# Performance work log

Hardware: AMD Instinct MI355X
Metric: run time of the kernel (lower is better)

The kernel has to match this reference:

```python
import jax, jax.numpy as jnp
import numpy as np

N_GROUPS = 32  # getGroupSize(.) assumed -> channels // 8 (or //24 for 3*ch) == 32 for ch=256
HEADS = 4


def group_norm(x, gamma, beta, groups=N_GROUPS, eps=1e-5):
    n, c = x.shape
    xg = x.reshape(n, groups, c // groups)
    mu = xg.mean(-1, keepdims=True)
    var = xg.var(-1, keepdims=True)
    xn = ((xg - mu) * jax.lax.rsqrt(var + eps)).reshape(n, c)
    return xn * gamma + beta


def setup_inputs():
    key = jax.random.key(0)
    N, E, CH, HID = 2000, 16000, 256, 256
    ks = jax.random.split(key, 24)

    def w(k, shape, s=0.02):
        return (jax.random.normal(k, shape) * s).astype(jnp.float32)

    inp = {
        'x': jax.random.normal(ks[0], (N, CH), jnp.float32),
        'edge_index': jax.random.randint(ks[1], (2, E), 0, N),
        'edge_attr': jax.random.normal(ks[2], (E, CH), jnp.float32),
        # edge_mlp: GN(3ch)+ReLU -> Linear(3ch,hid) -> GN(hid)+ReLU -> Linear(hid,ch)
        'gn_e1_g': jnp.ones((3 * CH,), jnp.float32), 'gn_e1_b': jnp.zeros((3 * CH,), jnp.float32),
        'We1': w(ks[3], (3 * CH, HID)), 'be1': jnp.zeros((HID,), jnp.float32),
        'gn_e2_g': jnp.ones((HID,), jnp.float32), 'gn_e2_b': jnp.zeros((HID,), jnp.float32),
        'We2': w(ks[4], (HID, CH)), 'be2': jnp.zeros((CH,), jnp.float32),
        # actN: GN(ch)+ReLU
        'gn_n_g': jnp.ones((CH,), jnp.float32), 'gn_n_b': jnp.zeros((CH,), jnp.float32),
        # multi-head attention projections
        'Wq': w(ks[5], (CH, CH)), 'bq': jnp.zeros((CH,), jnp.float32),
        'Wk': w(ks[6], (CH, CH)), 'bk': jnp.zeros((CH,), jnp.float32),
        'Wv': w(ks[7], (CH, CH)), 'bv': jnp.zeros((CH,), jnp.float32),
        'Wo': w(ks[8], (CH, CH)), 'bo': jnp.zeros((CH,), jnp.float32),
        # node_mlp: Linear(2ch,hid) -> GN(hid)+ReLU -> Linear(hid,ch)
        'Wn1': w(ks[9], (2 * CH, HID)), 'bn1': jnp.zeros((HID,), jnp.float32),
        'gn_n2_g': jnp.ones((HID,), jnp.float32), 'gn_n2_b': jnp.zeros((HID,), jnp.float32),
        'Wn2': w(ks[10], (HID, CH)), 'bn2': jnp.zeros((CH,), jnp.float32),
    }
    return inp


def reference(x, edge_index, edge_attr,
              gn_e1_g, gn_e1_b, We1, be1, gn_e2_g, gn_e2_b, We2, be2,
              gn_n_g, gn_n_b, Wq, bq, Wk, bk, Wv, bv, Wo, bo,
              Wn1, bn1, gn_n2_g, gn_n2_b, Wn2, bn2):
    row, col = edge_index[0], edge_index[1]
    N, ch = x.shape
    E = edge_attr.shape[0]
    dk = ch // HEADS

    # ---- edge model: cat(src, tgt, e) -> GN/ReLU -> Lin -> GN/ReLU -> Lin (+res) ----
    e_in = jnp.concatenate([x[row], x[col], edge_attr], axis=1)  # [E, 3ch]
    h = jax.nn.relu(group_norm(e_in, gn_e1_g, gn_e1_b))
    h = h @ We1 + be1
    h = jax.nn.relu(group_norm(h, gn_e2_g, gn_e2_b))
    e_out = h @ We2 + be2 + edge_attr  # [E, ch]

    # ---- node model: dense-masked MHA, queries=nodes, keys/values=edges ----
    mask = jnp.zeros((N, E), x.dtype).at[col, jnp.arange(E)].set(1.0)  # scatter adjacency
    q = (x @ Wq + bq).reshape(N, HEADS, dk)
    k = (e_out @ Wk + bk).reshape(E, HEADS, dk)
    v = (e_out @ Wv + bv).reshape(E, HEADS, dk)
    scores = jnp.einsum('nhd,ehd->hne', q, k) / jnp.sqrt(jnp.float32(dk))  # [H, N, E]
    scores = jnp.where(mask[None] > 0, scores, jnp.float32(-1e9))
    attn = jax.nn.softmax(scores, axis=-1)
    g = jnp.einsum('hne,ehd->nhd', attn, v).reshape(N, ch) @ Wo + bo  # [N, ch]

    xa = jax.nn.relu(group_norm(x, gn_n_g, gn_n_b))
    h = jnp.concatenate([xa, g], axis=1) @ Wn1 + bn1  # thinker='cat'
    h = jax.nn.relu(group_norm(h, gn_n2_g, gn_n2_b))
    n_out = h @ Wn2 + bn2 + x  # residual

    return n_out, e_out
```

## Files before the change

### kernel.cpp

```cpp
#include <hip/hip_runtime.h>
#include <hip/hip_bf16.h>
#include <stdint.h>
#include <math.h>

#define CH 256

typedef __attribute__((ext_vector_type(8)))  short short8;
typedef __attribute__((ext_vector_type(16))) short short16;
typedef __attribute__((ext_vector_type(4)))  float f32x4;

#define GL2LDS16(g, l) __builtin_amdgcn_global_load_lds(                       \
    (const __attribute__((address_space(1))) void*)(g),                        \
    (__attribute__((address_space(3))) void*)(l), 16, 0, 0)

__device__ inline short f2bf(float f) {
    __hip_bfloat16 h = __float2bfloat16(f);
    short s;
    __builtin_memcpy(&s, &h, 2);
    return s;
}

__device__ inline float bf2f(short s) {
    unsigned u = ((unsigned)(unsigned short)s) << 16;
    float f;
    __builtin_memcpy(&f, &u, 4);
    return f;
}

__device__ inline float warp_sum64(float v) {
    v += __shfl_xor(v, 32, 64);
    v += __shfl_xor(v, 16, 64);
    v += __shfl_xor(v, 8, 64);
    v += __shfl_xor(v, 4, 64);
    v += __shfl_xor(v, 2, 64);
    v += __shfl_xor(v, 1, 64);
    return v;
}

__device__ inline float warp_max64(float v) {
    v = fmaxf(v, __shfl_xor(v, 32, 64));
    v = fmaxf(v, __shfl_xor(v, 16, 64));
    v = fmaxf(v, __shfl_xor(v, 8, 64));
    v = fmaxf(v, __shfl_xor(v, 4, 64));
    v = fmaxf(v, __shfl_xor(v, 2, 64));
    v = fmaxf(v, __shfl_xor(v, 1, 64));
    return v;
}

struct GArgs {
    const short* A; const short* Bt; const float* bias; const float* res;
    float* C; short* Cbf;
    const float* gamma; const float* beta; float* vbar;
    int M, K, Nc, ldc, coff;
    const short* A2; const short* Bt2; const float* bias2; short* Cbf2;
    int M2, Nc2, y_split;
    const short* xbf; const short* eabf; const int* rowi; const int* coli;
    const float* mu; const float* rs; const float* vg; const float* vbt;
    int* cursor; int* elist;
    const int* counts; int* offsets; int Nn;
};

template <int BM, int BN, int AMODE, int EPI, int DUAL, int VB, int FILL,
          int SCAN = 0, int PAN2 = 0>
__global__ __launch_bounds__(256) void mfma_gemm(GArgs g)
{
    constexpr int BK = 64;
    constexpr int AK = AMODE ? (BK + 8) : BK;
    constexpr int HM = BM / 2, HN = BN / 2;
    constexpr int FM = HM / 16, FN = HN / 16;
    constexpr int PA = BM / 32;
    constexpr int PB = BN / 32;
    constexpr int NP2 = PAN2 ? 2 : 1;
    __shared__ short As[BM * AK];
    __shared__ short Bs[NP2 * BN * BK];
    __shared__ int sidx[AMODE ? 2 * BM : 1];

    const short* A = g.A; const short* Bt = g.Bt;
    const float* bias = g.bias; const float* res = g.res;
    float* C = g.C; short* Cbf = g.Cbf;
    int M = g.M, ldc = g.ldc, co = g.coff;
    const int K = g.K;
    int by = blockIdx.y, bx = blockIdx.x;

    if constexpr (SCAN) {
        if (by == (int)gridDim.y - 1) {
            const int t0 = threadIdx.x;
            if (bx == 0) {
                int* ss = (int*)As;
                int base8 = t0 * 8;
                int loc[8]; int srun = 0;
                #pragma unroll
                for (int j = 0; j < 8; j++) {
                    int idx = base8 + j;
                    int c = (idx < g.Nn) ? g.counts[idx] : 0;
                    loc[j] = srun; srun += c;
                }
                ss[t0] = srun;
                __syncthreads();
                for (int off = 1; off < 256; off <<= 1) {
                    int v = (t0 >= off) ? ss[t0 - off] : 0;
                    __syncthreads();
                    ss[t0] += v;
                    __syncthreads();
                }
                int excl = (t0 > 0) ? ss[t0 - 1] : 0;
                #pragma unroll
                for (int j = 0; j < 8; j++) {
                    int idx = base8 + j;
                    if (idx < g.Nn) {
                        int v = excl + loc[j];
                        g.offsets[idx] = v;
                        g.cursor[idx]  = v;
                    }
                }
                if (t0 == 255) g.offsets[g.Nn] = ss[255];
            }
            return;
        }
    }

    bool qrole = false;
    if constexpr (DUAL) {
        if (by >= g.y_split) {
            by -= g.y_split;
            if (bx * BN >= g.Nc2) return;
            qrole = true;
            A = g.A2; Bt = g.Bt2; bias = g.bias2; Cbf = g.Cbf2;
            C = nullptr; res = nullptr;
            M = g.M2; ldc = g.Nc2; co = 0;
        }
    }

    const int t = threadIdx.x;
    const int wave = t >> 6, lane = t & 63;
    const int q = lane >> 4, l16 = lane & 15;
    const int row0 = by * BM;
    const int col0 = bx * BN;
    const int wm = wave & 1, wn = wave >> 1;

    if constexpr (AMODE) {
        if (t < BM) {
            int gr = row0 + t; if (gr >= M) gr = M - 1;
            sidx[t] = g.rowi[gr];
            sidx[BM + t] = g.coli[gr];
        }
        __syncthreads();
    }

    if constexpr (FILL) {
        if (!qrole && bx == 0 && t < BM) {
            int rg = row0 + t;
            if (rg < M) {
                int c = g.coli[rg];
                int p = atomicAdd(&g.cursor[c], 1);
                g.elist[p] = rg;
            }
        }
    }

    f32x4 acc[NP2][FM][FN];
    #pragma unroll
    for (int p2 = 0; p2 < NP2; p2++)
        #pragma unroll
        for (int i = 0; i < FM; i++)
            #pragma unroll
            for (int j = 0; j < FN; j++) acc[p2][i][j] = (f32x4){0.f, 0.f, 0.f, 0.f};

    for (int k0 = 0; k0 < K; k0 += BK) {
        if constexpr (AMODE == 1) {
            int reg = k0 >> 8;
            int rloc = t >> 3;
            int c8 = (t & 7) * 8;
            int pos = k0 + c8;
            int G = pos / 24;
            float4 ga  = *(const float4*)&g.vg[pos];
            float4 ga2 = *(const float4*)&g.vg[pos + 4];
            float4 gb  = *(const float4*)&g.vbt[pos];
            float4 gb2 = *(const float4*)&g.vbt[pos + 4];
            int off = pos & 255;
            #pragma unroll
            for (int p = 0; p < BM / 32; p++) {
                int r2 = p * 32 + rloc;
                int e = row0 + r2; if (e >= M) e = M - 1;
                const short* srow;
                if (reg == 0)      srow = g.xbf + (size_t)sidx[r2] * CH;
                else if (reg == 1) srow = g.xbf + (size_t)sidx[BM + r2] * CH;
                else               srow = g.eabf + (size_t)e * CH;
                short8 v8 = *(const short8*)&srow[off];
                float mm = g.mu[(size_t)e * 32 + G];
                float rr = g.rs[(size_t)e * 32 + G];
                short8 o;
                o[0] = f2bf(fmaxf((bf2f(v8[0]) - mm) * rr * ga.x + gb.x, 0.f));
                o[1] = f2bf(fmaxf((bf2f(v8[1]) - mm) * rr * ga.y + gb.y, 0.f));
                o[2] = f2bf(fmaxf((bf2f(v8[2]) - mm) * rr * ga.z + gb.z, 0.f));
                o[3] = f2bf(fmaxf((bf2f(v8[3]) - mm) * rr * ga.w + gb.w, 0.f));
                o[4] = f2bf(fmaxf((bf2f(v8[4]) - mm) * rr * ga2.x + gb2.x, 0.f));
                o[5] = f2bf(fmaxf((bf2f(v8[5]) - mm) * rr * ga2.y + gb2.y, 0.f));
                o[6] = f2bf(fmaxf((bf2f(v8[6]) - mm) * rr * ga2.z + gb2.z, 0.f));
                o[7] = f2bf(fmaxf((bf2f(v8[7]) - mm) * rr * ga2.w + gb2.w, 0.f));
                *(short8*)&As[r2 * AK + c8] = o;
            }
        } else {
            #pragma unroll
            for (int p = 0; p < PA; p++) {
                int chunk = p * 256 + t;
                int r = chunk >> 3;
                int cs = (((chunk & 7) ^ (r & 7)) * 8);
                int gr = row0 + r; if (gr >= M) gr = M - 1;
                const short* gsrc = A + (size_t)gr * K + k0 + cs;
                short* ldst = &As[(p * 256 + wave * 64) * 8];
                GL2LDS16(gsrc, ldst);
            }
        }
        #pragma unroll
        for (int p2 = 0; p2 < NP2; p2++) {
            if (!(PAN2 && p2 == 1 && qrole)) {
                #pragma unroll
                for (int p = 0; p < PB; p++) {
                    int chunk = p * 256 + t;
                    int r = chunk >> 3;
                    int cs = (((chunk & 7) ^ (r & 7)) * 8);
                    const short* gsrc = Bt + (size_t)(col0 + p2 * 256 + r) * K + k0 + cs;
                    short* ldst = &Bs[p2 * BN * BK + (p * 256 + wave * 64) * 8];
                    GL2LDS16(gsrc, ldst);
                }
            }
        }
        __syncthreads();
        #pragma unroll
        for (int ks = 0; ks < 2; ks++) {
            short8 af[FM];
            #pragma unroll
            for (int mi = 0; mi < FM; mi++) {
                int R = wm * HM + mi * 16 + l16;
                if constexpr (AMODE == 1)
                    af[mi] = *(const short8*)&As[R * AK + ks * 32 + q * 8];
                else {
                    int slot = ((ks * 4 + q) ^ (R & 7)) * 8;
                    af[mi] = *(const short8*)&As[R * BK + slot];
                }
            }
            #pragma unroll
            for (int p2 = 0; p2 < NP2; p2++) {
                if (!(PAN2 && p2 == 1 && qrole)) {
                    short8 bfr[FN];
                    #pragma unroll
                    for (int ni = 0; ni < FN; ni++) {
                        int R = wn * HN + ni * 16 + l16;
                        int slot = ((ks * 4 + q) ^ (R & 7)) * 8;
                        bfr[ni] = *(const short8*)&Bs[p2 * BN * BK + R * BK + slot];
                    }
                    #pragma unroll
                    for (int mi = 0; mi < FM; mi++)
                        #pragma unroll
                        for (int ni = 0; ni < FN; ni++)
                            acc[p2][mi][ni] = __builtin_amdgcn_mfma_f32_16x16x32_bf16(
                                af[mi], bfr[ni], acc[p2][mi][ni], 0, 0, 0);
                }
            }
        }
        __syncthreads();
    }

    #pragma unroll
    for (int p2 = 0; p2 < NP2; p2++) {
        if (PAN2 && p2 == 1 && qrole) continue;
        #pragma unroll
        for (int ni = 0; ni < FN; ni++) {
            int cg = col0 + p2 * 256 + wn * HN + ni * 16 + l16;
            float bv = bias[cg];
            if constexpr (EPI == 1) {
                float ga = g.gamma[cg], be = g.beta[cg];
                #pragma unroll
                for (int mi = 0; mi < FM; mi++) {
                    #pragma unroll
                    for (int r = 0; r < 4; r++) {
                        float v = acc[p2][mi][ni][r] + bv;
                        float s = v, sq = v * v;
                        s += __shfl_xor(s, 1, 64);  sq += __shfl_xor(sq, 1, 64);
                        s += __shfl_xor(s, 2, 64);  sq += __shfl_xor(sq, 2, 64);
                        s += __shfl_xor(s, 4, 64);  sq += __shfl_xor(sq, 4, 64);
                        float mean = s * 0.125f;
                        float var = sq * 0.125f - mean * mean;
                        float o = fmaxf((v - mean) * rsqrtf(var + 1e-5f) * ga + be, 0.f);
                        int rg = row0 + wm * HM + mi * 16 + q * 4 + r;
                        if (rg < M) Cbf[(size_t)rg * ldc + co + cg] = f2bf(o);
                    }
                }
            } else {
                #pragma unroll
                for (int mi = 0; mi < FM; mi++) {
                    #pragma unroll
                    for (int r = 0; r < 4; r++) {
                        int rg = row0 + wm * HM + mi * 16 + q * 4 + r;
                        if (rg < M) {
                            float v = acc[p2][mi][ni][r] + bv;
                            if (res) v += res[(size_t)rg * ldc + co + cg];
                            if (C)   C[(size_t)rg * ldc + co + cg] = v;
                            if (Cbf) Cbf[(size_t)rg * ldc + co + cg] = f2bf(v);
                        }
                    }
                }
                if constexpr (VB) {
                    bool vpanel = PAN2 ? (p2 == 1) : (!qrole && cg >= 256);
                    if (vpanel) {
                        float part = 0.f;
                        #pragma unroll
                        for (int mi = 0; mi < FM; mi++)
                            #pragma unroll
                            for (int r = 0; r < 4; r++) {
                                int rg = row0 + wm * HM + mi * 16 + q * 4 + r;
                                if (rg < M) part += acc[p2][mi][ni][r] + bv;
                            }
                        part += __shfl_xor(part, 16, 64);
                        part += __shfl_xor(part, 32, 64);
                        if (q == 0) atomicAdd(&g.vbar[cg - 256], part);
                    }
                }
            }
        }
    }
}

struct PrepPack {
    const float* wsrc[8];
    short* wdst[8];
    int wK[8];
    int wstart[8];
    int NW, NP;
    const float* x;
    short* x_bf;
    short* cat_bf;
    float2* xs;
    const float* gng;
    const float* gnb;
    float* vbar;
    const float* bk;
    const float* bv;
    float* bkv;
    int* counts;
    int N;
};

__global__ __launch_bounds__(256) void prep_kernel(PrepPack p)
{
    int bid = blockIdx.x;
    int t = threadIdx.x;
    if (bid < p.NW) {
        int m = 0;
        #pragma unroll
        for (int i = 1; i < 8; i++) if (bid >= p.wstart[i]) m = i;
        int k0 = (bid - p.wstart[m]) * 16;
        const float* src = p.wsrc[m];
        short16 o;
        #pragma unroll
        for (int j = 0; j < 16; j++) o[j] = f2bf(src[(size_t)(k0 + j) * 256 + t]);
        *(short16*)(p.wdst[m] + (size_t)t * p.wK[m] + k0) = o;
        return;
    }
    if (bid >= p.NW + p.NP) {
        int i = (bid - p.NW - p.NP) * 256 + t;
        if (i < p.N) p.counts[i] = 0;
        return;
    }
    int pb = bid - p.NW;
    if (pb == 0) {
        p.vbar[t] = 0.f;
        p.bkv[t] = p.bk[t];
        p.bkv[256 + t] = p.bv[t];
    }
    int r = pb * 8 + (t >> 5);
    int g = t & 31;
    if (r >= p.N) return;
    size_t xb = (size_t)r * CH + g * 8;
    float4 a = *(const float4*)&p.x[xb];
    float4 b = *(const float4*)&p.x[xb + 4];
    short8 xr;
    xr[0] = f2bf(a.x); xr[1] = f2bf(a.y); xr[2] = f2bf(a.z); xr[3] = f2bf(a.w);
    xr[4] = f2bf(b.x); xr[5] = f2bf(b.y); xr[6] = f2bf(b.z); xr[7] = f2bf(b.w);
    *(short8*)&p.x_bf[xb] = xr;
    float s  = a.x + a.y + a.z + a.w + b.x + b.y + b.z + b.w;
    float s2 = a.x*a.x + a.y*a.y + a.z*a.z + a.w*a.w
             + b.x*b.x + b.y*b.y + b.z*b.z + b.w*b.w;
    p.xs[(size_t)r * 32 + g] = make_float2(s, s2);
    float m = s * 0.125f;
    float var = s2 * 0.125f - m * m;
    float rsd = rsqrtf(var + 1e-5f);
    float4 g0 = *(const float4*)&p.gng[g * 8];
    float4 g1 = *(const float4*)&p.gng[g * 8 + 4];
    float4 b0 = *(const float4*)&p.gnb[g * 8];
    float4 b1 = *(const float4*)&p.gnb[g * 8 + 4];
    short8 o;
    o[0] = f2bf(fmaxf((a.x - m) * rsd * g0.x + b0.x, 0.f));
    o[1] = f2bf(fmaxf((a.y - m) * rsd * g0.y + b0.y, 0.f));
    o[2] = f2bf(fmaxf((a.z - m) * rsd * g0.z + b0.z, 0.f));
    o[3] = f2bf(fmaxf((a.w - m) * rsd * g0.w + b0.w, 0.f));
    o[4] = f2bf(fmaxf((b.x - m) * rsd * g1.x + b1.x, 0.f));
    o[5] = f2bf(fmaxf((b.y - m) * rsd * g1.y + b1.y, 0.f));
    o[6] = f2bf(fmaxf((b.z - m) * rsd * g1.z + b1.z, 0.f));
    o[7] = f2bf(fmaxf((b.w - m) * rsd * g1.w + b1.w, 0.f));
    *(short8*)&p.cat_bf[(size_t)r * (2 * CH) + g * 8] = o;
}

__global__ __launch_bounds__(256) void estats_kernel(
    const float* __restrict__ eattr, const int* __restrict__ rowi,
    const int* __restrict__ coli, const float2* __restrict__ xs,
    float* __restrict__ mu, float* __restrict__ rs,
    short* __restrict__ eabf, int* __restrict__ counts, int E)
{
    __shared__ float2 ea[8][32];
    int t = threadIdx.x;
    int slot = t >> 5, g = t & 31;
    int e = blockIdx.x * 8 + slot;
    float4 a = *(const float4*)&eattr[(size_t)e * CH + g * 8];
    float4 b = *(const float4*)&eattr[(size_t)e * CH + g * 8 + 4];
    short8 o8;
    o8[0] = f2bf(a.x); o8[1] = f2bf(a.y); o8[2] = f2bf(a.z); o8[3] = f2bf(a.w);
    o8[4] = f2bf(b.x); o8[5] = f2bf(b.y); o8[6] = f2bf(b.z); o8[7] = f2bf(b.w);
    *(short8*)&eabf[(size_t)e * CH + g * 8] = o8;
    float s  = a.x + a.y + a.z + a.w + b.x + b.y + b.z + b.w;
    float s2 = a.x*a.x + a.y*a.y + a.z*a.z + a.w*a.w
             + b.x*b.x + b.y*b.y + b.z*b.z + b.w*b.w;
    ea[slot][g] = make_float2(s, s2);
    int r = rowi[e], c = coli[e];
    if (g == 0) atomicAdd(&counts[c], 1);
    __syncthreads();
    float S = 0.f, S2 = 0.f;
    #pragma unroll
    for (int j = 0; j < 3; j++) {
        int b3 = 3 * g + j;
        int src = b3 >> 5, idx = b3 & 31;
        float2 v;
        if (src == 0)      v = xs[(size_t)r * 32 + idx];
        else if (src == 1) v = xs[(size_t)c * 32 + idx];
        else               v = ea[slot][idx];
        S += v.x; S2 += v.y;
    }
    float m = S * (1.f / 24.f);
    float var = S2 * (1.f / 24.f) - m * m;
    mu[(size_t)e * 32 + g] = m;
    rs[(size_t)e * 32 + g] = rsqrtf(var + 1e-5f);
}

__global__ __launch_bounds__(256) void attn_kernel(
    const short* __restrict__ qb, const short* __restrict__ kvb,
    const int* __restrict__ offsets, const int* __restrict__ elist,
    const float* __restrict__ vbar, short* __restrict__ g_bf, int N, int E)
{
    __shared__ int eidx[64];
    __shared__ float scl[4 * 64];
    int n = blockIdx.x;
    int wave = threadIdx.x >> 6;
    int lane = threadIdx.x & 63;
    int s0 = offsets[n], s1 = offsets[n + 1];
    float q0 = bf2f(qb[(size_t)n * CH + lane]);
    float q1 = bf2f(qb[(size_t)n * CH + 64 + lane]);
    float q2 = bf2f(qb[(size_t)n * CH + 128 + lane]);
    float q3 = bf2f(qb[(size_t)n * CH + 192 + lane]);
    float out = 0.f, m = -INFINITY, l = 0.f;
    for (int base = s0; base < s1; base += 64) {
        int cn = s1 - base; if (cn > 64) cn = 64;
        if (wave == 0 && lane < cn) eidx[lane] = elist[base + lane];
        __syncthreads();
        for (int j = wave; j < cn; j += 4) {
            int e = eidx[j];
            const short* kr = kvb + (size_t)e * 512;
            float d0 = warp_sum64(q0 * bf2f(kr[lane]));
            float d1 = warp_sum64(q1 * bf2f(kr[64 + lane]));
            float d2 = warp_sum64(q2 * bf2f(kr[128 + lane]));
            float d3 = warp_sum64(q3 * bf2f(kr[192 + lane]));
            if (lane == 0) {
                scl[j]       = d0 * 0.125f;
                scl[64 + j]  = d1 * 0.125f;
                scl[128 + j] = d2 * 0.125f;
                scl[192 + j] = d3 * 0.125f;
            }
        }
        __syncthreads();
        float s = (lane < cn) ? scl[wave * 64 + lane] : -INFINITY;
        float mc = warp_max64(s);
        float nm = fmaxf(m, mc);
        float scale = __expf(m - nm);
        float pp = (lane < cn) ? __expf(s - nm) : 0.f;
        float ps = warp_sum64(pp);
        l = l * scale + ps;
        out *= scale;
        m = nm;
        for (int i = 0; i < cn; i++) {
            float pi = __shfl(pp, i, 64);
            int ei = eidx[i];
            out += pi * bf2f(kvb[(size_t)ei * 512 + 256 + wave * 64 + lane]);
        }
        __syncthreads();
    }
    float res;
    if (s1 > s0) res = out / l;
    else         res = vbar[wave * 64 + lane] * (1.f / (float)E);
    g_bf[(size_t)n * CH + wave * 64 + lane] = f2bf(res);
}

extern "C" void kernel_launch(void* const* d_in, const int* in_sizes, int n_in,
                              void* d_out, int out_size, void* d_ws, size_t ws_size,
                              hipStream_t stream)
{
    const float* x       = (const float*)d_in[0];
    const int*   ei      = (const int*)d_in[1];
    const float* eattr   = (const float*)d_in[2];
    const float* gn_e1_g = (const float*)d_in[3];
    const float* gn_e1_b = (const float*)d_in[4];
    const float* We1     = (const float*)d_in[5];
    const float* be1     = (const float*)d_in[6];
    const float* gn_e2_g = (const float*)d_in[7];
    const float* gn_e2_b = (const float*)d_in[8];
    const float* We2     = (const float*)d_in[9];
    const float* be2     = (const float*)d_in[10];
    const float* gn_n_g  = (const float*)d_in[11];
    const float* gn_n_b  = (const float*)d_in[12];
    const float* Wq      = (const float*)d_in[13];
    const float* bq      = (const float*)d_in[14];
    const float* Wk      = (const float*)d_in[15];
    const float* bk      = (const float*)d_in[16];
    const float* Wv      = (const float*)d_in[17];
    const float* bv      = (const float*)d_in[18];
    const float* Wo      = (const float*)d_in[19];
    const float* bo      = (const float*)d_in[20];
    const float* Wn1     = (const float*)d_in[21];
    const float* bn1     = (const float*)d_in[22];
    const float* gn_n2_g = (const float*)d_in[23];
    const float* gn_n2_b = (const float*)d_in[24];
    const float* Wn2     = (const float*)d_in[25];
    const float* bn2     = (const float*)d_in[26];

    const int N = in_sizes[0] / CH;
    const int E = in_sizes[2] / CH;

    float* nout = (float*)d_out;
    float* eout = (float*)d_out + (size_t)N * CH;

    char* base = (char*)d_ws;
    short* kv_bf  = (short*)base; base += (size_t)E * 512 * 2;
    short* h2_bf  = (short*)base; base += (size_t)E * CH * 2;
    short* eo_bf  = (short*)base; base += (size_t)E * CH * 2;
    short* eabf   = (short*)base; base += (size_t)E * CH * 2;
    short* q_bf   = (short*)base; base += (size_t)N * CH * 2;
    short* g_bf   = (short*)base; base += (size_t)N * CH * 2;
    short* cat_bf = (short*)base; base += (size_t)N * 2 * CH * 2;
    short* hn_bf  = (short*)base; base += (size_t)N * CH * 2;
    short* x_bf   = (short*)base; base += (size_t)N * CH * 2;
    float2* xs    = (float2*)base; base += (size_t)N * 32 * 8;
    float* mub    = (float*)base; base += (size_t)E * 32 * 4;
    float* rsb    = (float*)base; base += (size_t)E * 32 * 4;
    float* vbar   = (float*)base; base += 1024;
    float* bkv    = (float*)base; base += 2048;
    short* We1t = (short*)base; base += (size_t)768 * 256 * 2;
    short* We2t = (short*)base; base += (size_t)256 * 256 * 2;
    short* Wqt  = (short*)base; base += (size_t)256 * 256 * 2;
    short* Wkvt = (short*)base; base += (size_t)512 * 256 * 2;
    short* Wot  = (short*)base; base += (size_t)256 * 256 * 2;
    short* Wn1t = (short*)base; base += (size_t)512 * 256 * 2;
    short* Wn2t = (short*)base; base += (size_t)256 * 256 * 2;
    int* counts  = (int*)base;
    int* offsets = counts + N;
    int* cursor  = offsets + (N + 1) + 3;
    int* elist   = cursor + N;

    const int* rowi = ei;
    const int* coli = ei + E;

    dim3 blk(256);

    PrepPack pp;
    const float* wsrc[8] = {We1, We2, Wq, Wk, Wv, Wo, Wn1, Wn2};
    short* wdst[8] = {We1t, We2t, Wqt, Wkvt, Wkvt + (size_t)256 * 256, Wot, Wn1t, Wn2t};
    const int wKd[8] = {768, 256, 256, 256, 256, 256, 512, 256};
    int acc = 0;
    for (int i = 0; i < 8; i++) {
        pp.wsrc[i] = wsrc[i]; pp.wdst[i] = wdst[i]; pp.wK[i] = wKd[i];
        pp.wstart[i] = acc; acc += wKd[i] / 16;
    }
    pp.NW = acc;
    pp.NP = (N + 7) / 8;
    pp.x = x; pp.x_bf = x_bf; pp.cat_bf = cat_bf; pp.xs = xs;
    pp.gng = gn_n_g; pp.gnb = gn_n_b;
    pp.vbar = vbar; pp.bk = bk; pp.bv = bv; pp.bkv = bkv;
    pp.counts = counts; pp.N = N;
    int nzero = (N + 255) / 256;
    prep_kernel<<<pp.NW + pp.NP + nzero, blk, 0, stream>>>(pp);

    estats_kernel<<<E / 8, blk, 0, stream>>>(eattr, rowi, coli, xs, mub, rsb,
                                             eabf, counts, E);

    GArgs ga = {};
    ga.Bt = We1t; ga.bias = be1; ga.Cbf = h2_bf;
    ga.gamma = gn_e2_g; ga.beta = gn_e2_b;
    ga.M = E; ga.K = 3 * CH; ga.Nc = CH; ga.ldc = CH; ga.coff = 0;
    ga.xbf = x_bf; ga.eabf = eabf; ga.rowi = rowi; ga.coli = coli;
    ga.mu = mub; ga.rs = rsb; ga.vg = gn_e1_g; ga.vbt = gn_e1_b;
    ga.counts = counts; ga.offsets = offsets; ga.cursor = cursor; ga.Nn = N;
    mfma_gemm<64, 64, 1, 1, 0, 0, 0, 1, 0><<<dim3(4, E / 64 + 1), blk, 0, stream>>>(ga);

    ga = {};
    ga.A = h2_bf; ga.Bt = We2t; ga.bias = be2; ga.res = eattr;
    ga.C = eout; ga.Cbf = eo_bf;
    ga.M = E; ga.K = CH; ga.Nc = CH; ga.ldc = CH; ga.coff = 0;
    mfma_gemm<64, 64, 0, 0, 0, 0, 0><<<dim3(4, E / 64), blk, 0, stream>>>(ga);

    ga = {};
    ga.A = eo_bf; ga.Bt = Wkvt; ga.bias = bkv; ga.Cbf = kv_bf; ga.vbar = vbar;
    ga.M = E; ga.K = CH; ga.Nc = 512; ga.ldc = 512; ga.coff = 0;
    ga.A2 = x_bf; ga.Bt2 = Wqt; ga.bias2 = bq; ga.Cbf2 = q_bf;
    ga.M2 = N; ga.Nc2 = CH; ga.y_split = E / 64;
    ga.coli = coli; ga.cursor = cursor; ga.elist = elist;
    mfma_gemm<64, 64, 0, 0, 1, 1, 1, 0, 1><<<dim3(4, E / 64 + (N + 63) / 64), blk, 0, stream>>>(ga);

    attn_kernel<<<N, blk, 0, stream>>>(q_bf, kv_bf, offsets, elist, vbar, g_bf, N, E);

    ga = {};
    ga.A = g_bf; ga.Bt = Wot; ga.bias = bo; ga.Cbf = cat_bf;
    ga.M = N; ga.K = CH; ga.Nc = CH; ga.ldc = 2 * CH; ga.coff = CH;
    mfma_gemm<32, 64, 0, 0, 0, 0, 0><<<dim3(4, (N + 31) / 32), blk, 0, stream>>>(ga);

    ga = {};
    ga.A = cat_bf; ga.Bt = Wn1t; ga.bias = bn1; ga.Cbf = hn_bf;
    ga.gamma = gn_n2_g; ga.beta = gn_n2_b;
    ga.M = N; ga.K = 2 * CH; ga.Nc = CH; ga.ldc = CH; ga.coff = 0;
    mfma_gemm<32, 64, 0, 1, 0, 0, 0><<<dim3(4, (N + 31) / 32), blk, 0, stream>>>(ga);

    ga = {};
    ga.A = hn_bf; ga.Bt = Wn2t; ga.bias = bn2; ga.res = x; ga.C = nout;
    ga.M = N; ga.K = CH; ga.Nc = CH; ga.ldc = CH; ga.coff = 0;
    mfma_gemm<32, 64, 0, 0, 0, 0, 0><<<dim3(4, (N + 31) / 32), blk, 0, stream>>>(ga);
}
```

Baseline: 238.1 us.

## Materialize normalized edge concat in stats kernel instead of gathering inside GEMM

Moves the gather of x[row], x[col] and edge_attr, plus the first GroupNorm+ReLU, out of the first edge GEMM's A-tile loader and into the edge stats kernel. The stats kernel now writes a bf16 [E,768] normalized input, and the GEMM loads it with the standard async global-to-LDS swizzled path. This drops the per-k-tile register-path gather and normalization from the GEMM and removes the mu/rs buffers. In exchange it writes and rereads a larger E*768 bf16 intermediate, about 24MB of extra traffic.

```diff
diff --git a/kernel.cpp b/kernel.cpp
--- a/kernel.cpp
+++ b/kernel.cpp
@@ -54,26 +54,23 @@
     int M, K, Nc, ldc, coff;
     const short* A2; const short* Bt2; const float* bias2; short* Cbf2;
     int M2, Nc2, y_split;
-    const short* xbf; const short* eabf; const int* rowi; const int* coli;
-    const float* mu; const float* rs; const float* vg; const float* vbt;
+    const int* coli;
     int* cursor; int* elist;
     const int* counts; int* offsets; int Nn;
 };
 
-template <int BM, int BN, int AMODE, int EPI, int DUAL, int VB, int FILL,
+template <int BM, int BN, int EPI, int DUAL, int VB, int FILL,
           int SCAN = 0, int PAN2 = 0>
 __global__ __launch_bounds__(256) void mfma_gemm(GArgs g)
 {
     constexpr int BK = 64;
-    constexpr int AK = AMODE ? (BK + 8) : BK;
     constexpr int HM = BM / 2, HN = BN / 2;
     constexpr int FM = HM / 16, FN = HN / 16;
     constexpr int PA = BM / 32;
     constexpr int PB = BN / 32;
     constexpr int NP2 = PAN2 ? 2 : 1;
-    __shared__ short As[BM * AK];
+    __shared__ short As[BM * BK];
     __shared__ short Bs[NP2 * BN * BK];
-    __shared__ int sidx[AMODE ? 2 * BM : 1];
 
     const short* A = g.A; const short* Bt = g.Bt;
     const float* bias = g.bias; const float* res = g.res;
@@ -138,15 +135,6 @@
     const int col0 = bx * BN;
     const int wm = wave & 1, wn = wave >> 1;
 
-    if constexpr (AMODE) {
-        if (t < BM) {
-            int gr = row0 + t; if (gr >= M) gr = M - 1;
-            sidx[t] = g.rowi[gr];
-            sidx[BM + t] = g.coli[gr];
-        }
-        __syncthreads();
-    }
-
     if constexpr (FILL) {
         if (!qrole && bx == 0 && t < BM) {
             int rg = row0 + t;
@@ -167,50 +155,15 @@
             for (int j = 0; j < FN; j++) acc[p2][i][j] = (f32x4){0.f, 0.f, 0.f, 0.f};
 
     for (int k0 = 0; k0 < K; k0 += BK) {
-        if constexpr (AMODE == 1) {
-            int reg = k0 >> 8;
-            int rloc = t >> 3;
-            int c8 = (t & 7) * 8;
-            int pos = k0 + c8;
-            int G = pos / 24;
-            float4 ga  = *(const float4*)&g.vg[pos];
-            float4 ga2 = *(const float4*)&g.vg[pos + 4];
-            float4 gb  = *(const float4*)&g.vbt[pos];
-            float4 gb2 = *(const float4*)&g.vbt[pos + 4];
-            int off = pos & 255;
-            #pragma unroll
-            for (int p = 0; p < BM / 32; p++) {
-                int r2 = p * 32 + rloc;
-                int e = row0 + r2; if (e >= M) e = M - 1;
-                const short* srow;
-                if (reg == 0)      srow = g.xbf + (size_t)sidx[r2] * CH;
-                else if (reg == 1) srow = g.xbf + (size_t)sidx[BM + r2] * CH;
-                else               srow = g.eabf + (size_t)e * CH;
-                short8 v8 = *(const short8*)&srow[off];
-                float mm = g.mu[(size_t)e * 32 + G];
-                float rr = g.rs[(size_t)e * 32 + G];
-                short8 o;
-                o[0] = f2bf(fmaxf((bf2f(v8[0]) - mm) * rr * ga.x + gb.x, 0.f));
-                o[1] = f2bf(fmaxf((bf2f(v8[1]) - mm) * rr * ga.y + gb.y, 0.f));
-                o[2] = f2bf(fmaxf((bf2f(v8[2]) - mm) * rr * ga.z + gb.z, 0.f));
-                o[3] = f2bf(fmaxf((bf2f(v8[3]) - mm) * rr * ga.w + gb.w, 0.f));
-                o[4] = f2bf(fmaxf((bf2f(v8[4]) - mm) * rr * ga2.x + gb2.x, 0.f));
-                o[5] = f2bf(fmaxf((bf2f(v8[5]) - mm) * rr * ga2.y + gb2.y, 0.f));
-                o[6] = f2bf(fmaxf((bf2f(v8[6]) - mm) * rr * ga2.z + gb2.z, 0.f));
-                o[7] = f2bf(fmaxf((bf2f(v8[7]) - mm) * rr * ga2.w + gb2.w, 0.f));
-                *(short8*)&As[r2 * AK + c8] = o;
-            }
-        } else {
-            #pragma unroll
-            for (int p = 0; p < PA; p++) {
-                int chunk = p * 256 + t;
-                int r = chunk >> 3;
-                int cs = (((chunk & 7) ^ (r & 7)) * 8);
-                int gr = row0 + r; if (gr >= M) gr = M - 1;
-                const short* gsrc = A + (size_t)gr * K + k0 + cs;
-                short* ldst = &As[(p * 256 + wave * 64) * 8];
-                GL2LDS16(gsrc, ldst);
-            }
+        #pragma unroll
+        for (int p = 0; p < PA; p++) {
+            int chunk = p * 256 + t;
+            int r = chunk >> 3;
+            int cs = (((chunk & 7) ^ (r & 7)) * 8);
+            int gr = row0 + r; if (gr >= M) gr = M - 1;
+            const short* gsrc = A + (size_t)gr * K + k0 + cs;
+            short* ldst = &As[(p * 256 + wave * 64) * 8];
+            GL2LDS16(gsrc, ldst);
         }
         #pragma unroll
         for (int p2 = 0; p2 < NP2; p2++) {
@@ -233,12 +186,8 @@
             #pragma unroll
             for (int mi = 0; mi < FM; mi++) {
                 int R = wm * HM + mi * 16 + l16;
-                if constexpr (AMODE == 1)
-                    af[mi] = *(const short8*)&As[R * AK + ks * 32 + q * 8];
-                else {
-                    int slot = ((ks * 4 + q) ^ (R & 7)) * 8;
-                    af[mi] = *(const short8*)&As[R * BK + slot];
-                }
+                int slot = ((ks * 4 + q) ^ (R & 7)) * 8;
+                af[mi] = *(const short8*)&As[R * BK + slot];
             }
             #pragma unroll
             for (int p2 = 0; p2 < NP2; p2++) {
@@ -405,19 +354,17 @@
 __global__ __launch_bounds__(256) void estats_kernel(
     const float* __restrict__ eattr, const int* __restrict__ rowi,
     const int* __restrict__ coli, const float2* __restrict__ xs,
-    float* __restrict__ mu, float* __restrict__ rs,
-    short* __restrict__ eabf, int* __restrict__ counts, int E)
+    const short* __restrict__ x_bf,
+    const float* __restrict__ g1v, const float* __restrict__ b1v,
+    short* __restrict__ e1n, int* __restrict__ counts, int E)
 {
     __shared__ float2 ea[8][32];
+    __shared__ float2 musr[8][32];
     int t = threadIdx.x;
     int slot = t >> 5, g = t & 31;
     int e = blockIdx.x * 8 + slot;
     float4 a = *(const float4*)&eattr[(size_t)e * CH + g * 8];
     float4 b = *(const float4*)&eattr[(size_t)e * CH + g * 8 + 4];
-    short8 o8;
-    o8[0] = f2bf(a.x); o8[1] = f2bf(a.y); o8[2] = f2bf(a.z); o8[3] = f2bf(a.w);
-    o8[4] = f2bf(b.x); o8[5] = f2bf(b.y); o8[6] = f2bf(b.z); o8[7] = f2bf(b.w);
-    *(short8*)&eabf[(size_t)e * CH + g * 8] = o8;
     float s  = a.x + a.y + a.z + a.w + b.x + b.y + b.z + b.w;
     float s2 = a.x*a.x + a.y*a.y + a.z*a.z + a.w*a.w
              + b.x*b.x + b.y*b.y + b.z*b.z + b.w*b.w;
@@ -438,8 +385,37 @@
     }
     float m = S * (1.f / 24.f);
     float var = S2 * (1.f / 24.f) - m * m;
-    mu[(size_t)e * 32 + g] = m;
-    rs[(size_t)e * 32 + g] = rsqrtf(var + 1e-5f);
+    musr[slot][g] = make_float2(m, rsqrtf(var + 1e-5f));
+    __syncthreads();
+    #pragma unroll
+    for (int seg = 0; seg < 3; seg++) {
+        int pos = seg * 256 + g * 8;
+        float2 ms = musr[slot][pos / 24];
+        float4 ga  = *(const float4*)&g1v[pos];
+        float4 ga2 = *(const float4*)&g1v[pos + 4];
+        float4 gb  = *(const float4*)&b1v[pos];
+        float4 gb2 = *(const float4*)&b1v[pos + 4];
+        float v0, v1, v2, v3, v4, v5, v6, v7;
+        if (seg == 2) {
+            v0 = a.x; v1 = a.y; v2 = a.z; v3 = a.w;
+            v4 = b.x; v5 = b.y; v6 = b.z; v7 = b.w;
+        } else {
+            const short* srow = x_bf + (size_t)(seg == 0 ? r : c) * CH + g * 8;
+            short8 v8 = *(const short8*)srow;
+            v0 = bf2f(v8[0]); v1 = bf2f(v8[1]); v2 = bf2f(v8[2]); v3 = bf2f(v8[3]);
+            v4 = bf2f(v8[4]); v5 = bf2f(v8[5]); v6 = bf2f(v8[6]); v7 = bf2f(v8[7]);
+        }
+        short8 o;
+        o[0] = f2bf(fmaxf((v0 - ms.x) * ms.y * ga.x  + gb.x,  0.f));
+        o[1] = f2bf(fmaxf((v1 - ms.x) * ms.y * ga.y  + gb.y,  0.f));
+        o[2] = f2bf(fmaxf((v2 - ms.x) * ms.y * ga.z  + gb.z,  0.f));
+        o[3] = f2bf(fmaxf((v3 - ms.x) * ms.y * ga.w  + gb.w,  0.f));
+        o[4] = f2bf(fmaxf((v4 - ms.x) * ms.y * ga2.x + gb2.x, 0.f));
+        o[5] = f2bf(fmaxf((v5 - ms.x) * ms.y * ga2.y + gb2.y, 0.f));
+        o[6] = f2bf(fmaxf((v6 - ms.x) * ms.y * ga2.z + gb2.z, 0.f));
+        o[7] = f2bf(fmaxf((v7 - ms.x) * ms.y * ga2.w + gb2.w, 0.f));
+        *(short8*)&e1n[(size_t)e * 768 + pos] = o;
+    }
 }
 
 __global__ __launch_bounds__(256) void attn_kernel(
@@ -541,15 +517,13 @@
     short* kv_bf  = (short*)base; base += (size_t)E * 512 * 2;
     short* h2_bf  = (short*)base; base += (size_t)E * CH * 2;
     short* eo_bf  = (short*)base; base += (size_t)E * CH * 2;
-    short* eabf   = (short*)base; base += (size_t)E * CH * 2;
+    short* e1n    = (short*)base; base += (size_t)E * 768 * 2;
     short* q_bf   = (short*)base; base += (size_t)N * CH * 2;
     short* g_bf   = (short*)base; base += (size_t)N * CH * 2;
     short* cat_bf = (short*)base; base += (size_t)N * 2 * CH * 2;
     short* hn_bf  = (short*)base; base += (size_t)N * CH * 2;
     short* x_bf   = (short*)base; base += (size_t)N * CH * 2;
     float2* xs    = (float2*)base; base += (size_t)N * 32 * 8;
-    float* mub    = (float*)base; base += (size_t)E * 32 * 4;
-    float* rsb    = (float*)base; base += (size_t)E * 32 * 4;
     float* vbar   = (float*)base; base += 1024;
     float* bkv    = (float*)base; base += 2048;
     short* We1t = (short*)base; base += (size_t)768 * 256 * 2;
@@ -587,23 +561,21 @@
     int nzero = (N + 255) / 256;
     prep_kernel<<<pp.NW + pp.NP + nzero, blk, 0, stream>>>(pp);
 
-    estats_kernel<<<E / 8, blk, 0, stream>>>(eattr, rowi, coli, xs, mub, rsb,
-                                             eabf, counts, E);
+    estats_kernel<<<E / 8, blk, 0, stream>>>(eattr, rowi, coli, xs, x_bf,
+                                             gn_e1_g, gn_e1_b, e1n, counts, E);
 
     GArgs ga = {};
-    ga.Bt = We1t; ga.bias = be1; ga.Cbf = h2_bf;
+    ga.A = e1n; ga.Bt = We1t; ga.bias = be1; ga.Cbf = h2_bf;
     ga.gamma = gn_e2_g; ga.beta = gn_e2_b;
     ga.M = E; ga.K = 3 * CH; ga.Nc = CH; ga.ldc = CH; ga.coff = 0;
-    ga.xbf = x_bf; ga.eabf = eabf; ga.rowi = rowi; ga.coli = coli;
-    ga.mu = mub; ga.rs = rsb; ga.vg = gn_e1_g; ga.vbt = gn_e1_b;
     ga.counts = counts; ga.offsets = offsets; ga.cursor = cursor; ga.Nn = N;
-    mfma_gemm<64, 64, 1, 1, 0, 0, 0, 1, 0><<<dim3(4, E / 64 + 1), blk, 0, stream>>>(ga);
+    mfma_gemm<64, 64, 1, 0, 0, 0, 1, 0><<<dim3(4, E / 64 + 1), blk, 0, stream>>>(ga);
 
     ga = {};
     ga.A = h2_bf; ga.Bt = We2t; ga.bias = be2; ga.res = eattr;
     ga.C = eout; ga.Cbf = eo_bf;
     ga.M = E; ga.K = CH; ga.Nc = CH; ga.ldc = CH; ga.coff = 0;
-    mfma_gemm<64, 64, 0, 0, 0, 0, 0><<<dim3(4, E / 64), blk, 0, stream>>>(ga);
+    mfma_gemm<64, 64, 0, 0, 0, 0><<<dim3(4, E / 64), blk, 0, stream>>>(ga);
 
     ga = {};
     ga.A = eo_bf; ga.Bt = Wkvt; ga.bias = bkv; ga.Cbf = kv_bf; ga.vbar = vbar;
@@ -611,23 +583,23 @@
     ga.A2 = x_bf; ga.Bt2 = Wqt; ga.bias2 = bq; ga.Cbf2 = q_bf;
     ga.M2 = N; ga.Nc2 = CH; ga.y_split = E / 64;
     ga.coli = coli; ga.cursor = cursor; ga.elist = elist;
-    mfma_gemm<64, 64, 0, 0, 1, 1, 1, 0, 1><<<dim3(4, E / 64 + (N + 63) / 64), blk, 0, stream>>>(ga);
+    mfma_gemm<64, 64, 0, 1, 1, 1, 0, 1><<<dim3(4, E / 64 + (N + 63) / 64), blk, 0, stream>>>(ga);
 
     attn_kernel<<<N, blk, 0, stream>>>(q_bf, kv_bf, offsets, elist, vbar, g_bf, N, E);
 
     ga = {};
     ga.A = g_bf; ga.Bt = Wot; ga.bias = bo; ga.Cbf = cat_bf;
     ga.M = N; ga.K = CH; ga.Nc = CH; ga.ldc = 2 * CH; ga.coff = CH;
-    mfma_gemm<32, 64, 0, 0, 0, 0, 0><<<dim3(4, (N + 31) / 32), blk, 0, stream>>>(ga);
+    mfma_gemm<32, 64, 0, 0, 0, 0><<<dim3(4, (N + 31) / 32), blk, 0, stream>>>(ga);
 
     ga = {};
     ga.A = cat_bf; ga.Bt = Wn1t; ga.bias = bn1; ga.Cbf = hn_bf;
     ga.gamma = gn_n2_g; ga.beta = gn_n2_b;
     ga.M = N; ga.K = 2 * CH; ga.Nc = CH; ga.ldc = CH; ga.coff = 0;
-    mfma_gemm<32, 64, 0, 1, 0, 0, 0><<<dim3(4, (N + 31) / 32), blk, 0, stream>>>(ga);
+    mfma_gemm<32, 64, 1, 0, 0, 0><<<dim3(4, (N + 31) / 32), blk, 0, stream>>>(ga);
 
     ga = {};
     ga.A = hn_bf; ga.Bt = Wn2t; ga.bias = bn2; ga.res = x; ga.C = nout;
     ga.M = N; ga.K = CH; ga.Nc = CH; ga.ldc = CH; ga.coff = 0;
-    mfma_gemm<32, 64, 0, 0, 0, 0, 0><<<dim3(4, (N + 31) / 32), blk, 0, stream>>>(ga);
-}
+    mfma_gemm<32, 64, 0, 0, 0, 0><<<dim3(4, (N + 31) / 32), blk, 0, stream>>>(ga);
+}
```

After: 233.2 us. 2.1% less time.
